# Optimization experiments

Measured on AMD Instinct MI355X. Metric: run time of the kernel, lower is better.

The kernel has to match this reference:

```python
import jax, jax.numpy as jnp
import numpy as np

# BEV projection config (from model_cfg.PROJECT_CFG)
PCR = np.array([0.0, -40.0, -3.0, 70.4, 40.0, 1.0], dtype=np.float32)
VOX = np.array([0.16, 0.16, 4.0], dtype=np.float32)
NX = int(round((PCR[3] - PCR[0]) / VOX[0]))  # 440
NY = int(round((PCR[4] - PCR[1]) / VOX[1]))  # 500
NVOX = NX * NY


def setup_inputs() -> dict:
    key = jax.random.key(0)
    ks = jax.random.split(key, 7)
    B, C, H, W = 2, 32, 32, 256
    fv = jax.random.normal(ks[0], (B, C, H, W), jnp.float32)
    lo = jnp.array([0.0, -40.0, -3.0], jnp.float32).reshape(1, 3, 1, 1)
    hi = jnp.array([70.4, 40.0, 1.0], jnp.float32).reshape(1, 3, 1, 1)

    def mk_pts(k1, k2):
        xyz = lo + jax.random.uniform(k1, (B, 3, H, W), jnp.float32) * (hi - lo)
        inten = jax.random.uniform(k2, (B, 1, H, W), jnp.float32)
        return jnp.concatenate([xyz, inten], axis=1)

    points_img = mk_pts(ks[1], ks[2])
    points_img_far = mk_pts(ks[3], ks[4])
    proj_masks = jax.random.randint(ks[5], (B, H, W), 0, 2).astype(jnp.int32)
    proj_masks_far = jax.random.randint(ks[6], (B, H, W), 0, 2).astype(jnp.int32)
    return {
        "fv_features": fv,
        "points_img": points_img,
        "points_img_far": points_img_far,
        "proj_masks": proj_masks,
        "proj_masks_far": proj_masks_far,
    }


def _bev_scatter(points, feats, valid):
    """Scatter-mean per-point features into the BEV grid.

    points: (M, 3), feats: (M, C), valid: (M,) bool. Invalid / out-of-range
    points go to an overflow bucket that is dropped.
    """
    ix = jnp.floor((points[:, 0] - PCR[0]) / VOX[0]).astype(jnp.int32)
    iy = jnp.floor((points[:, 1] - PCR[1]) / VOX[1]).astype(jnp.int32)
    inb = (ix >= 0) & (ix < NX) & (iy >= 0) & (iy < NY)
    inb = inb & (points[:, 2] >= PCR[2]) & (points[:, 2] < PCR[5])
    ok = valid & inb
    seg = jnp.where(ok, iy * NX + ix, NVOX)
    fsum = jax.ops.segment_sum(jnp.where(ok[:, None], feats, 0.0), seg,
                               num_segments=NVOX + 1)
    cnt = jax.ops.segment_sum(ok.astype(feats.dtype), seg,
                              num_segments=NVOX + 1)
    mean = fsum[:NVOX] / jnp.maximum(cnt[:NVOX], 1.0)[:, None]
    return mean.reshape(NY, NX, -1).transpose(2, 0, 1)  # (C, NY, NX)


def reference(fv_features, points_img, points_img_far, proj_masks, proj_masks_far):
    B, C, H, W = fv_features.shape
    N = H * W
    feats = fv_features.transpose(0, 2, 3, 1).reshape(B, N, C)
    pts = points_img[:, :3].transpose(0, 2, 3, 1).reshape(B, N, 3)
    ptsf = points_img_far[:, :3].transpose(0, 2, 3, 1).reshape(B, N, 3)
    m = proj_masks.reshape(B, N) > 0      # valid near points (knowns)
    mf = proj_masks_far.reshape(B, N) > 0  # valid far points (unknowns)

    # three_nn: squared distances from far points to valid near points
    d2 = jnp.sum((ptsf[:, :, None, :] - pts[:, None, :, :]) ** 2, axis=-1)  # (B,N,N)
    d2 = jnp.where(m[:, None, :], d2, jnp.inf)
    neg, idx = jax.lax.top_k(-d2, 3)  # (B,N,3) three nearest
    dist = -neg
    dist_recip = 1.0 / (dist + 1e-8)
    weight = dist_recip / jnp.sum(dist_recip, axis=-1, keepdims=True)  # (B,N,3)

    # three_interpolate: weighted gather of near features
    gathered = jnp.take_along_axis(
        feats, idx.reshape(B, N * 3)[:, :, None], axis=1).reshape(B, N, 3, C)
    interp = jnp.sum(gathered * weight[..., None], axis=2)  # (B,N,C)

    # cat([features, interpolated]), cat([points, points_far]) -> BEV scatter
    all_pts = jnp.concatenate([pts, ptsf], axis=1)       # (B, 2N, 3)
    all_feats = jnp.concatenate([feats, interp], axis=1)  # (B, 2N, C)
    all_valid = jnp.concatenate([m, mf], axis=1)          # (B, 2N)
    bev = jax.vmap(_bev_scatter)(all_pts, all_feats, all_valid)  # (B,C,NY,NX)
    return bev
```

## Files before the change

### kernel.cpp

```cpp
#include <hip/hip_runtime.h>

#define BB   2
#define CC   32
#define NN   8192
#define N2   (2 * NN)
#define NXv  440
#define NYv  500
#define NVOXv (NXv * NYv)

#define SPLIT 16
#define FPB   16

#define INSERT3(dd, jj)                                            \
    if ((dd) < d2) {                                               \
        if ((dd) < d1) {                                           \
            d2 = d1; i2 = i1;                                      \
            if ((dd) < d0) { d1 = d0; i1 = i0; d0 = (dd); i0 = (jj); } \
            else           { d1 = (dd); i1 = (jj); }               \
        } else { d2 = (dd); i2 = (jj); }                           \
    }

__global__ __launch_bounds__(256) void k_prep(
    const float* __restrict__ fv,
    const float* __restrict__ pim,
    const float* __restrict__ pimf,
    const int*   __restrict__ pm,
    const int*   __restrict__ pmf,
    float*       __restrict__ F,
    int*         __restrict__ head,
    int*         __restrict__ nxt,
    float4*      __restrict__ cand,
    int*         __restrict__ counters,
    float4*      __restrict__ fcand)
{
    __shared__ float tile[CC][64 + 1];
    int b  = blockIdx.y;
    int i0 = blockIdx.x * 64;
    int t  = threadIdx.x;

    const float* f = fv + (size_t)b * CC * NN;
    int il = t & 63, cb = t >> 6;
#pragma unroll
    for (int p = 0; p < 8; ++p) {
        int c = cb + p * 4;
        tile[c][il] = f[(size_t)c * NN + i0 + il];
    }
    __syncthreads();
    float* o = F + ((size_t)b * N2 + i0) * CC;
    int c2 = t & 31, ib = t >> 5;
#pragma unroll
    for (int p = 0; p < 8; ++p) {
        int il2 = ib + p * 8;
        o[(size_t)il2 * CC + c2] = tile[c2][il2];
    }

    if (t < 64) {
        int i = i0 + t;

        {
            float x = pimf[(b * 4 + 0) * NN + i];
            float y = pimf[(b * 4 + 1) * NN + i];
            float z = pimf[(b * 4 + 2) * NN + i];
            if (pmf[b * NN + i] > 0) {
                int ix = (int)floorf((x - 0.0f)  / 0.16f);
                int iy = (int)floorf((y + 40.0f) / 0.16f);
                if (ix >= 0 && ix < NXv && iy >= 0 && iy < NYv &&
                    z >= -3.0f && z < 1.0f) {
                    int vox = iy * NXv + ix;
                    int pos = atomicAdd(&counters[2 + b], 1) + 1;
                    fcand[b * NN + pos] = make_float4(x, y, z, __int_as_float(vox));
                }
            }
        }

        if (pm[b * NN + i] > 0) {
            float x = pim[(b * 4 + 0) * NN + i];
            float y = pim[(b * 4 + 1) * NN + i];
            float z = pim[(b * 4 + 2) * NN + i];
            int pos = atomicAdd(&counters[b], 1) + 1;
            cand[b * NN + pos] = make_float4(x, y, z, __int_as_float(i));

            int ix = (int)floorf((x - 0.0f)  / 0.16f);
            int iy = (int)floorf((y + 40.0f) / 0.16f);
            if (ix >= 0 && ix < NXv && iy >= 0 && iy < NYv &&
                z >= -3.0f && z < 1.0f) {
                int vox = iy * NXv + ix;
                nxt[b * N2 + i] = atomicExch(&head[b * NVOXv + vox], i);
            }
        }
    }
}

__global__ __launch_bounds__(256) void k_far(
    const float4* __restrict__ cand,
    const int*    __restrict__ counters,
    const float4* __restrict__ fcand,
    float*        __restrict__ F,
    int*          __restrict__ head,
    int*          __restrict__ nxt)
{
    int b  = blockIdx.y;
    int nf = counters[2 + b] + 1;
    int e0 = blockIdx.x * FPB;
    if (e0 >= nf) return;

    int tid = threadIdx.x;
    int sub = tid & (SPLIT - 1);
    int e   = e0 + (tid >> 4);
    if (e >= nf) return;

    float4 fp = fcand[b * NN + e];
    float x = fp.x, y = fp.y, z = fp.z;
    int vox = __float_as_int(fp.w);

    int nc = counters[b] + 1;
    const float4* cb = cand + b * NN;

    float d0 = __builtin_inff(), d1 = __builtin_inff(), d2 = __builtin_inff();
    int   i0 = 0, i1 = 0, i2 = 0;

    int k = sub;
    for (; k + 48 < nc; k += 64) {
        float4 pa = cb[k];
        float4 pb = cb[k + 16];
        float4 pc = cb[k + 32];
        float4 pd = cb[k + 48];
        float dxa = x - pa.x, dya = y - pa.y, dza = z - pa.z;
        float dxb = x - pb.x, dyb = y - pb.y, dzb = z - pb.z;
        float dxc = x - pc.x, dyc = y - pc.y, dzc = z - pc.z;
        float dxd = x - pd.x, dyd = y - pd.y, dzd = z - pd.z;
        float da = dxa * dxa + dya * dya + dza * dza;
        float db = dxb * dxb + dyb * dyb + dzb * dzb;
        float dc = dxc * dxc + dyc * dyc + dzc * dzc;
        float dd = dxd * dxd + dyd * dyd + dzd * dzd;
        int ia = __float_as_int(pa.w);
        int ib = __float_as_int(pb.w);
        int ic = __float_as_int(pc.w);
        int id = __float_as_int(pd.w);
        INSERT3(da, ia);
        INSERT3(db, ib);
        INSERT3(dc, ic);
        INSERT3(dd, id);
    }
    for (; k < nc; k += SPLIT) {
        float4 p = cb[k];
        float dx = x - p.x, dy = y - p.y, dz = z - p.z;
        float d  = dx * dx + dy * dy + dz * dz;
        int  ii  = __float_as_int(p.w);
        INSERT3(d, ii);
    }

#pragma unroll
    for (int off = 1; off < SPLIT; off <<= 1) {
        float m0 = __shfl_xor(d0, off), m1 = __shfl_xor(d1, off), m2 = __shfl_xor(d2, off);
        int   g0 = __shfl_xor(i0, off), g1 = __shfl_xor(i1, off), g2 = __shfl_xor(i2, off);
        INSERT3(m0, g0);
        INSERT3(m1, g1);
        INSERT3(m2, g2);
    }

    float r0 = 1.0f / (d0 + 1e-8f);
    float r1 = 1.0f / (d1 + 1e-8f);
    float r2 = 1.0f / (d2 + 1e-8f);
    float s  = r0 + r1 + r2;
    float w0 = r0 / s, w1 = r1 / s, w2 = r2 / s;

    const float* fb = F + ((size_t)b * N2 << 5);
    float va = w0 * fb[((size_t)i0 << 5) + sub] +
               w1 * fb[((size_t)i1 << 5) + sub] +
               w2 * fb[((size_t)i2 << 5) + sub];
    float vb = w0 * fb[((size_t)i0 << 5) + sub + 16] +
               w1 * fb[((size_t)i1 << 5) + sub + 16] +
               w2 * fb[((size_t)i2 << 5) + sub + 16];
    size_t row = ((size_t)b * N2 + NN + e) << 5;
    F[row + sub]      = va;
    F[row + sub + 16] = vb;

    if (sub == 0)
        nxt[b * N2 + NN + e] = atomicExch(&head[b * NVOXv + vox], NN + e);
}

__global__ __launch_bounds__(256) void k_final(
    const float* __restrict__ F,
    const int*   __restrict__ head,
    const int*   __restrict__ nxt,
    float*       __restrict__ out)
{
    __shared__ float tile[CC][64 + 1];
    int b  = blockIdx.y;
    int v0 = blockIdx.x * 64;
    int t  = threadIdx.x;

    int vl = t >> 2, cq = (t & 3) * 8;
    int v  = v0 + vl;
    float acc[8] = {0, 0, 0, 0, 0, 0, 0, 0};
    if (v < NVOXv) {
        int p = head[b * NVOXv + v];
        int n = 0;
        while (p >= 0) {
            const float* f = F + (((size_t)b * N2 + p) << 5) + cq;
            float4 a0 = *(const float4*)f;
            float4 a1 = *(const float4*)(f + 4);
            acc[0] += a0.x; acc[1] += a0.y; acc[2] += a0.z; acc[3] += a0.w;
            acc[4] += a1.x; acc[5] += a1.y; acc[6] += a1.z; acc[7] += a1.w;
            ++n;
            p = nxt[b * N2 + p];
        }
        if (n > 1) {
            float cf = (float)n;
#pragma unroll
            for (int u = 0; u < 8; ++u) acc[u] /= cf;
        }
    }
#pragma unroll
    for (int u = 0; u < 8; ++u) tile[cq + u][vl] = acc[u];
    __syncthreads();

    int c = t >> 3, vb = (t & 7) * 8;
    if (v0 + vb < NVOXv) {
        float* o = out + (size_t)b * CC * NVOXv + (size_t)c * NVOXv + v0 + vb;
        *(float4*)(o)     = make_float4(tile[c][vb + 0], tile[c][vb + 1],
                                        tile[c][vb + 2], tile[c][vb + 3]);
        *(float4*)(o + 4) = make_float4(tile[c][vb + 4], tile[c][vb + 5],
                                        tile[c][vb + 6], tile[c][vb + 7]);
    }
}

extern "C" void kernel_launch(void* const* d_in, const int* in_sizes, int n_in,
                              void* d_out, int out_size, void* d_ws, size_t ws_size,
                              hipStream_t stream)
{
    const float* fv   = (const float*)d_in[0];
    const float* pim  = (const float*)d_in[1];
    const float* pimf = (const float*)d_in[2];
    const int*   pm   = (const int*)d_in[3];
    const int*   pmf  = (const int*)d_in[4];
    float* out = (float*)d_out;

    const size_t headB = (size_t)BB * NVOXv * sizeof(int);
    const size_t nxtB  = (size_t)BB * N2 * sizeof(int);
    const size_t candB = (size_t)BB * NN * sizeof(float4);
    const size_t FB    = (size_t)BB * N2 * CC * sizeof(float);

    char* ws = (char*)d_ws;
    int* counters = (int*)ws;
    size_t off = 256;
    int*    head  = (int*)(ws + off);   off += headB;
    int*    nxt   = (int*)(ws + off);   off += nxtB;
    float4* cand  = (float4*)(ws + off); off += candB;
    float4* fcand = (float4*)(ws + off); off += candB;
    float*  F     = (float*)(ws + off);  off += FB;
    (void)ws_size;

    hipMemsetAsync(d_ws, 0xFF, 256 + headB, stream);

    dim3 blk(256);
    dim3 g1(NN / 64, BB);
    k_prep<<<g1, blk, 0, stream>>>(fv, pim, pimf, pm, pmf,
                                   F, head, nxt, cand, counters, fcand);

    dim3 g2(NN / FPB, BB);
    k_far<<<g2, blk, 0, stream>>>(cand, counters, fcand, F, head, nxt);

    dim3 g3((NVOXv + 63) / 64, BB);
    k_final<<<g3, blk, 0, stream>>>(F, head, nxt, out);
}
```

Baseline: 139.8 us.

## Split each far-point kNN scan across a full wavefront with branchless top-3 insert

Each far point's nearest-neighbour scan is now split across 64 lanes (a full wavefront) instead of 16, with 4 far points per block instead of 16. The branchy top-3 insertion is replaced by a select-based version to avoid divergence. The interpolation writes one channel per lane for the first 32 lanes. The goal is shorter per-lane scan loops and less divergence, in exchange for more shuffle-reduction steps, four times as many blocks, and idle lanes in the epilogue.

New measurement: 124.9 us. 10.6% less time.

```diff
diff --git a/kernel.cpp b/kernel.cpp
--- a/kernel.cpp
+++ b/kernel.cpp
@@ -8,17 +8,19 @@
 #define NYv  500
 #define NVOXv (NXv * NYv)
 
-#define SPLIT 16
-#define FPB   16
-
-#define INSERT3(dd, jj)                                            \
-    if ((dd) < d2) {                                               \
-        if ((dd) < d1) {                                           \
-            d2 = d1; i2 = i1;                                      \
-            if ((dd) < d0) { d1 = d0; i1 = i0; d0 = (dd); i0 = (jj); } \
-            else           { d1 = (dd); i1 = (jj); }               \
-        } else { d2 = (dd); i2 = (jj); }                           \
-    }
+#define SPLIT 64
+#define FPB   4
+
+#define INS3(dd, jj) do {                                          \
+    bool c0 = (dd) < d0, c1 = (dd) < d1, c2 = (dd) < d2;           \
+    float nd2 = c1 ? d1 : (c2 ? (dd) : d2);                        \
+    int   ni2 = c1 ? i1 : (c2 ? (jj) : i2);                        \
+    float nd1 = c0 ? d0 : (c1 ? (dd) : d1);                        \
+    int   ni1 = c0 ? i0 : (c1 ? (jj) : i1);                        \
+    float nd0 = c0 ? (dd) : d0;                                    \
+    int   ni0 = c0 ? (jj) : i0;                                    \
+    d0 = nd0; d1 = nd1; d2 = nd2; i0 = ni0; i1 = ni1; i2 = ni2;    \
+} while (0)
 
 __global__ __launch_bounds__(256) void k_prep(
     const float* __restrict__ fv,
@@ -106,7 +108,7 @@
 
     int tid = threadIdx.x;
     int sub = tid & (SPLIT - 1);
-    int e   = e0 + (tid >> 4);
+    int e   = e0 + (tid >> 6);
     if (e >= nf) return;
 
     float4 fp = fcand[b * NN + e];
@@ -120,11 +122,11 @@
     int   i0 = 0, i1 = 0, i2 = 0;
 
     int k = sub;
-    for (; k + 48 < nc; k += 64) {
+    for (; k + 192 < nc; k += 256) {
         float4 pa = cb[k];
-        float4 pb = cb[k + 16];
-        float4 pc = cb[k + 32];
-        float4 pd = cb[k + 48];
+        float4 pb = cb[k + 64];
+        float4 pc = cb[k + 128];
+        float4 pd = cb[k + 192];
         float dxa = x - pa.x, dya = y - pa.y, dza = z - pa.z;
         float dxb = x - pb.x, dyb = y - pb.y, dzb = z - pb.z;
         float dxc = x - pc.x, dyc = y - pc.y, dzc = z - pc.z;
@@ -137,26 +139,26 @@
         int ib = __float_as_int(pb.w);
         int ic = __float_as_int(pc.w);
         int id = __float_as_int(pd.w);
-        INSERT3(da, ia);
-        INSERT3(db, ib);
-        INSERT3(dc, ic);
-        INSERT3(dd, id);
+        INS3(da, ia);
+        INS3(db, ib);
+        INS3(dc, ic);
+        INS3(dd, id);
     }
     for (; k < nc; k += SPLIT) {
         float4 p = cb[k];
         float dx = x - p.x, dy = y - p.y, dz = z - p.z;
         float d  = dx * dx + dy * dy + dz * dz;
         int  ii  = __float_as_int(p.w);
-        INSERT3(d, ii);
+        INS3(d, ii);
     }
 
 #pragma unroll
     for (int off = 1; off < SPLIT; off <<= 1) {
         float m0 = __shfl_xor(d0, off), m1 = __shfl_xor(d1, off), m2 = __shfl_xor(d2, off);
         int   g0 = __shfl_xor(i0, off), g1 = __shfl_xor(i1, off), g2 = __shfl_xor(i2, off);
-        INSERT3(m0, g0);
-        INSERT3(m1, g1);
-        INSERT3(m2, g2);
+        INS3(m0, g0);
+        INS3(m1, g1);
+        INS3(m2, g2);
     }
 
     float r0 = 1.0f / (d0 + 1e-8f);
@@ -165,16 +167,13 @@
     float s  = r0 + r1 + r2;
     float w0 = r0 / s, w1 = r1 / s, w2 = r2 / s;
 
-    const float* fb = F + ((size_t)b * N2 << 5);
-    float va = w0 * fb[((size_t)i0 << 5) + sub] +
-               w1 * fb[((size_t)i1 << 5) + sub] +
-               w2 * fb[((size_t)i2 << 5) + sub];
-    float vb = w0 * fb[((size_t)i0 << 5) + sub + 16] +
-               w1 * fb[((size_t)i1 << 5) + sub + 16] +
-               w2 * fb[((size_t)i2 << 5) + sub + 16];
-    size_t row = ((size_t)b * N2 + NN + e) << 5;
-    F[row + sub]      = va;
-    F[row + sub + 16] = vb;
+    if (sub < CC) {
+        const float* fb = F + ((size_t)b * N2 << 5);
+        float v = w0 * fb[((size_t)i0 << 5) + sub] +
+                  w1 * fb[((size_t)i1 << 5) + sub] +
+                  w2 * fb[((size_t)i2 << 5) + sub];
+        F[(((size_t)b * N2 + NN + e) << 5) + sub] = v;
+    }
 
     if (sub == 0)
         nxt[b * N2 + NN + e] = atomicExch(&head[b * NVOXv + vox], NN + e);
```
